# Kernel optimization log

Measured on AMD Instinct MI355X. Metric: run time of the kernel, lower is better.

Reference implementation:

```python
import jax, jax.numpy as jnp
import numpy as np

N_NODES = 50000
N_EDGES = 800000
N_GRAPHS = 64
D_IN = 768
D_HID = 256


def gcn_conv(x, src, dst, W, b, n_nodes):
    """PyG GCNConv: symmetric-normalized aggregation with self-loops.
    out = D^{-1/2} (A + I) D^{-1/2} (x @ W) + b
    """
    h = x @ W  # [N, C_out]
    # degree from target nodes, counting the implicit self-loop (+1)
    deg = jax.ops.segment_sum(jnp.ones((src.shape[0],), h.dtype), dst,
                              num_segments=n_nodes) + 1.0
    dinv = jax.lax.rsqrt(deg)  # deg >= 1 always (self-loop)
    norm = (dinv[src] * dinv[dst])[:, None]  # [E, 1]
    agg = jax.ops.segment_sum(h[src] * norm, dst, num_segments=n_nodes)
    # self-loop contribution: norm_ii = dinv_i^2
    agg = agg + (dinv * dinv)[:, None] * h
    return agg + b


def global_mean_pool(x, batch, n_graphs):
    s = jax.ops.segment_sum(x, batch, num_segments=n_graphs)
    cnt = jax.ops.segment_sum(jnp.ones((x.shape[0],), x.dtype), batch,
                              num_segments=n_graphs)
    return s / jnp.maximum(cnt, 1.0)[:, None]


def setup_inputs() -> dict:
    key = jax.random.key(0)
    ks = jax.random.split(key, 12)
    x = jax.random.normal(ks[0], (N_NODES, D_IN), jnp.float32)
    edge_index = jax.random.randint(ks[1], (2, N_EDGES), 0, N_NODES, jnp.int64)
    batch = jnp.sort(jax.random.randint(ks[2], (N_NODES,), 0, N_GRAPHS, jnp.int64))
    def glorot(k, shape):
        lim = np.sqrt(6.0 / (shape[0] + shape[1]))
        return jax.random.uniform(k, shape, jnp.float32, -lim, lim)
    return {
        "x": x, "edge_index": edge_index, "batch": batch,
        "W1": glorot(ks[3], (D_IN, D_HID)), "b1": jnp.zeros((D_HID,), jnp.float32),
        "W2": glorot(ks[4], (D_HID, D_HID)), "b2": jnp.zeros((D_HID,), jnp.float32),
        "W3": glorot(ks[5], (D_HID, D_HID)), "b3": jnp.zeros((D_HID,), jnp.float32),
        "Wl": glorot(ks[6], (D_HID, D_IN)), "bl": jnp.zeros((D_IN,), jnp.float32),
    }


def reference(x, edge_index, batch, W1, b1, W2, b2, W3, b3, Wl, bl):
    src, dst = edge_index[0], edge_index[1]
    n = x.shape[0]
    # dropout is identity in eval mode
    h = jax.nn.relu(gcn_conv(x, src, dst, W1, b1, n))
    h = jax.nn.relu(gcn_conv(h, src, dst, W2, b2, n))
    h = gcn_conv(h, src, dst, W3, b3, n)
    g = global_mean_pool(h, batch, N_GRAPHS)  # [G, D_HID]
    return g @ Wl + bl  # [G, D_IN]
```

## Files before the change

### kernel.cpp

```cpp
#include <hip/hip_runtime.h>
#include <hip/hip_bf16.h>

#define D_IN 768
#define D_HID 256

typedef __attribute__((ext_vector_type(8))) short short8;
typedef __attribute__((ext_vector_type(4))) float f32x4;

__device__ inline float b2f(unsigned short u) {
    unsigned x = ((unsigned)u) << 16;
    union { unsigned u; float f; } c; c.u = x; return c.f;
}


__global__ void k_count(const int* __restrict__ dst, int* __restrict__ deg, int E) {
    int i = blockIdx.x * 256 + threadIdx.x;
    if (i < E) atomicAdd(&deg[dst[i]], 1);
}

__global__ void k_dinv(const int* __restrict__ deg, float* __restrict__ dinv, int N) {
    int i = blockIdx.x * 256 + threadIdx.x;
    if (i < N) dinv[i] = rsqrtf((float)deg[i] + 1.0f);
}

__global__ __launch_bounds__(1024) void k_scan(const int* __restrict__ deg,
                                               int* __restrict__ row_ptr, int N) {
    __shared__ int wsum[16];
    __shared__ int carry_s;
    int t = threadIdx.x;
    int lane = t & 63, wid = t >> 6;
    if (t == 0) carry_s = 0;
    __syncthreads();
    for (int base = 0; base < N; base += 1024) {
        int i = base + t;
        int v = (i < N) ? deg[i] : 0;
        int s = v;
        #pragma unroll
        for (int d = 1; d < 64; d <<= 1) {
            int tmp = __shfl_up(s, d);
            if (lane >= d) s += tmp;
        }
        if (lane == 63) wsum[wid] = s;
        __syncthreads();
        if (wid == 0 && lane < 16) {
            int ws = wsum[lane];
            #pragma unroll
            for (int d = 1; d < 16; d <<= 1) {
                int tmp = __shfl_up(ws, d);
                if (lane >= d) ws += tmp;
            }
            wsum[lane] = ws;
        }
        __syncthreads();
        int carry = carry_s;
        int woff = (wid > 0) ? wsum[wid - 1] : 0;
        if (i < N) row_ptr[i] = carry + woff + s - v;
        __syncthreads();
        if (t == 0) carry_s = carry + wsum[15];
        __syncthreads();
    }
    if (t == 0) row_ptr[N] = carry_s;
}

__global__ void k_fill(const int* __restrict__ src, const int* __restrict__ dst,
                       const int* __restrict__ row_ptr, int* __restrict__ wptr,
                       int* __restrict__ csr_src, int E) {
    int i = blockIdx.x * 256 + threadIdx.x;
    if (i < E) {
        int d = dst[i];
        int w = atomicAdd(&wptr[d], 1);
        csr_src[row_ptr[d] + w] = src[i];
    }
}

__global__ void k_bounds(const int* __restrict__ batch, int* __restrict__ cnt,
                         int* __restrict__ offg, int N, int G) {
    int g = threadIdx.x;
    if (g >= G) return;
    auto lower = [&](int key) {
        int lo = 0, hi = N;
        while (lo < hi) {
            int mid = (lo + hi) >> 1;
            if (batch[mid] < key) lo = mid + 1; else hi = mid;
        }
        return lo;
    };
    int lo = lower(g);
    int hi = lower(g + 1);
    offg[g] = lo;
    cnt[g] = hi - lo;
}

__global__ void k_prep_B(const float* __restrict__ B, short* __restrict__ Bp, int K) {
    int t = blockIdx.x * 256 + threadIdx.x;
    if (t >= K * 256) return;
    int k = t >> 8, n = t & 255;
    float v = B[(size_t)k * 256 + n];
    __hip_bfloat16 h = __float2bfloat16(v);
    float hf = __bfloat162float(h);
    float r = v - hf;
    __hip_bfloat16 l = __float2bfloat16(r);
    int c = k >> 5, q = (k >> 3) & 3, j = k & 7;
    size_t oh = ((size_t)(c * 2 + 0) * 4 + q) * 2048 + n * 8 + j;
    size_t ol = ((size_t)(c * 2 + 1) * 4 + q) * 2048 + n * 8 + j;
    Bp[oh] = *(short*)&h;
    Bp[ol] = *(short*)&l;
}

__global__ __launch_bounds__(256) void k_gemm_mfma(const float* __restrict__ A,
                                                   const short* __restrict__ Bp,
                                                   unsigned short* __restrict__ C,
                                                   int M, int K) {
    __shared__ short Bs[16384];
    int t = threadIdx.x;
    int lane = t & 63, w = t >> 6;
    int ln = lane & 15, q = lane >> 4;
    int bm = blockIdx.x * 64;
    int m_g = bm + w * 16 + ln;
    bool valid = m_g < M;
    const float* Arow = A + (size_t)(valid ? m_g : 0) * K;

    f32x4 acc[16];
    #pragma unroll
    for (int i = 0; i < 16; ++i) acc[i] = (f32x4){0.f, 0.f, 0.f, 0.f};

    int nchunks = K >> 5;
    for (int c = 0; c < nchunks; ++c) {
        __syncthreads();
        {
            const short* srcp = Bp + (size_t)c * 16384;
            #pragma unroll
            for (int i = 0; i < 8; ++i) {
                int s = (t + i * 256) * 8;
                *(short8*)&Bs[s] = *(const short8*)&srcp[s];
            }
        }
        float av[8];
        if (valid) {
            float4 v0 = *(const float4*)&Arow[c * 32 + q * 8];
            float4 v1 = *(const float4*)&Arow[c * 32 + q * 8 + 4];
            av[0] = v0.x; av[1] = v0.y; av[2] = v0.z; av[3] = v0.w;
            av[4] = v1.x; av[5] = v1.y; av[6] = v1.z; av[7] = v1.w;
        } else {
            #pragma unroll
            for (int i = 0; i < 8; ++i) av[i] = 0.f;
        }
        short8 a_hi, a_lo;
        #pragma unroll
        for (int i = 0; i < 8; ++i) {
            __hip_bfloat16 h = __float2bfloat16(av[i]);
            float hf = __bfloat162float(h);
            __hip_bfloat16 l = __float2bfloat16(av[i] - hf);
            a_hi[i] = *(short*)&h;
            a_lo[i] = *(short*)&l;
        }
        __syncthreads();
        #pragma unroll
        for (int tt = 0; tt < 16; ++tt) {
            short8 b_hi = *(const short8*)&Bs[(0 * 4 + q) * 2048 + (tt * 16 + ln) * 8];
            short8 b_lo = *(const short8*)&Bs[(1 * 4 + q) * 2048 + (tt * 16 + ln) * 8];
            acc[tt] = __builtin_amdgcn_mfma_f32_16x16x32_bf16(a_hi, b_hi, acc[tt], 0, 0, 0);
            acc[tt] = __builtin_amdgcn_mfma_f32_16x16x32_bf16(a_hi, b_lo, acc[tt], 0, 0, 0);
            acc[tt] = __builtin_amdgcn_mfma_f32_16x16x32_bf16(a_lo, b_hi, acc[tt], 0, 0, 0);
        }
    }
    #pragma unroll
    for (int tt = 0; tt < 16; ++tt) {
        #pragma unroll
        for (int r = 0; r < 4; ++r) {
            int row = bm + w * 16 + q * 4 + r;
            if (row < M) {
                __hip_bfloat16 h = __float2bfloat16(acc[tt][r]);
                C[(size_t)row * 256 + tt * 16 + ln] = *(unsigned short*)&h;
            }
        }
    }
}

template <int RELU>
__global__ __launch_bounds__(256) void k_agg(const unsigned short* __restrict__ hin,
                                             float* __restrict__ hout,
                                             const int* __restrict__ row_ptr,
                                             const int* __restrict__ csr_src,
                                             const float* __restrict__ dinv,
                                             const float* __restrict__ bias, int N) {
    int w = threadIdx.x >> 6;
    int lane = threadIdx.x & 63;
    int row = blockIdx.x * 4 + w;
    if (row >= N) return;
    int c4 = lane * 4;
    int s = row_ptr[row], e = row_ptr[row + 1];
    float a0 = 0.f, a1 = 0.f, a2 = 0.f, a3 = 0.f;
    int j = s;
    for (; j + 4 <= e; j += 4) {
        int u0 = csr_src[j], u1 = csr_src[j + 1], u2 = csr_src[j + 2], u3 = csr_src[j + 3];
        float d0 = dinv[u0], d1 = dinv[u1], d2 = dinv[u2], d3 = dinv[u3];
        ushort4 v0 = *(const ushort4*)&hin[(size_t)u0 * 256 + c4];
        ushort4 v1 = *(const ushort4*)&hin[(size_t)u1 * 256 + c4];
        ushort4 v2 = *(const ushort4*)&hin[(size_t)u2 * 256 + c4];
        ushort4 v3 = *(const ushort4*)&hin[(size_t)u3 * 256 + c4];
        a0 += d0 * b2f(v0.x) + d1 * b2f(v1.x) + d2 * b2f(v2.x) + d3 * b2f(v3.x);
        a1 += d0 * b2f(v0.y) + d1 * b2f(v1.y) + d2 * b2f(v2.y) + d3 * b2f(v3.y);
        a2 += d0 * b2f(v0.z) + d1 * b2f(v1.z) + d2 * b2f(v2.z) + d3 * b2f(v3.z);
        a3 += d0 * b2f(v0.w) + d1 * b2f(v1.w) + d2 * b2f(v2.w) + d3 * b2f(v3.w);
    }
    for (; j < e; ++j) {
        int u = csr_src[j];
        float d = dinv[u];
        ushort4 v = *(const ushort4*)&hin[(size_t)u * 256 + c4];
        a0 += d * b2f(v.x); a1 += d * b2f(v.y); a2 += d * b2f(v.z); a3 += d * b2f(v.w);
    }
    float di = dinv[row];
    float dii = di * di;
    ushort4 vs = *(const ushort4*)&hin[(size_t)row * 256 + c4];
    float4 bb = *(const float4*)&bias[c4];
    a0 = a0 * di + dii * b2f(vs.x) + bb.x;
    a1 = a1 * di + dii * b2f(vs.y) + bb.y;
    a2 = a2 * di + dii * b2f(vs.z) + bb.z;
    a3 = a3 * di + dii * b2f(vs.w) + bb.w;
    if (RELU) {
        a0 = fmaxf(a0, 0.f); a1 = fmaxf(a1, 0.f);
        a2 = fmaxf(a2, 0.f); a3 = fmaxf(a3, 0.f);
    }
    *(float4*)&hout[(size_t)row * 256 + c4] = make_float4(a0, a1, a2, a3);
}

__global__ __launch_bounds__(256) void k_pool(const float* __restrict__ h,
                                              const int* __restrict__ cnt,
                                              const int* __restrict__ offg,
                                              float* __restrict__ g) {
    int gi = blockIdx.x, slice = blockIdx.y;
    int c = threadIdx.x;
    int start = offg[gi], n = cnt[gi];
    int per = (n + (int)gridDim.y - 1) / (int)gridDim.y;
    int r0 = slice * per;
    int r1 = min(n, r0 + per);
    float acc = 0.f;
    for (int r = r0; r < r1; ++r) acc += h[(size_t)(start + r) * D_HID + c];
    if (r1 > r0) atomicAdd(&g[gi * D_HID + c], acc);
}

__global__ __launch_bounds__(256) void k_final(const float* __restrict__ g,
                                               const int* __restrict__ cnt,
                                               const float* __restrict__ Wl,
                                               const float* __restrict__ bl,
                                               float* __restrict__ out) {
    __shared__ float gs[D_HID];
    int t = threadIdx.x;
    int gi = blockIdx.y;
    int c = blockIdx.x * 256 + t;
    float inv = 1.0f / (float)max(cnt[gi], 1);
    gs[t] = g[gi * D_HID + t] * inv;
    __syncthreads();
    float acc = bl[c];
    #pragma unroll 8
    for (int k = 0; k < D_HID; ++k) acc = fmaf(gs[k], Wl[(size_t)k * D_IN + c], acc);
    out[(size_t)gi * D_IN + c] = acc;
}


extern "C" void kernel_launch(void* const* d_in, const int* in_sizes, int n_in,
                              void* d_out, int out_size, void* d_ws, size_t ws_size,
                              hipStream_t stream) {
    const float* x     = (const float*)d_in[0];
    const int*   ei    = (const int*)d_in[1];
    const int*   batch = (const int*)d_in[2];
    const float* W1 = (const float*)d_in[3];
    const float* b1 = (const float*)d_in[4];
    const float* W2 = (const float*)d_in[5];
    const float* b2 = (const float*)d_in[6];
    const float* W3 = (const float*)d_in[7];
    const float* b3 = (const float*)d_in[8];
    const float* Wl = (const float*)d_in[9];
    const float* bl = (const float*)d_in[10];
    float* out = (float*)d_out;

    int N = in_sizes[2];
    int E = in_sizes[1] / 2;
    int G = out_size / D_IN;
    const int* srcp = ei;
    const int* dstp = ei + E;

    char* ws = (char*)d_ws;
    size_t o = 0;
    auto alloc = [&](size_t bytes) -> char* {
        char* p = ws + o;
        o += (bytes + 255) & ~(size_t)255;
        return p;
    };
    int*   deg     = (int*)alloc((size_t)N * 4);
    int*   wptr    = (int*)alloc((size_t)N * 4);
    int*   row_ptr = (int*)alloc((size_t)(N + 1) * 4);
    int*   cnt     = (int*)alloc((size_t)G * 4);
    int*   offg    = (int*)alloc((size_t)G * 4);
    int*   csr_src = (int*)alloc((size_t)E * 4);
    float* dinv    = (float*)alloc((size_t)N * 4);
    float* gbuf    = (float*)alloc((size_t)G * D_HID * 4);
    unsigned short* hA = (unsigned short*)alloc((size_t)N * D_HID * 2);
    float* hB      = (float*)alloc((size_t)N * D_HID * 4);
    short* Bp1     = (short*)alloc((size_t)D_IN * 512 * 2);
    short* Bp2     = (short*)alloc((size_t)D_HID * 512 * 2);
    short* Bp3     = (short*)alloc((size_t)D_HID * 512 * 2);

    hipMemsetAsync(deg, 0, (size_t)N * 4, stream);
    hipMemsetAsync(wptr, 0, (size_t)N * 4, stream);
    hipMemsetAsync(gbuf, 0, (size_t)G * D_HID * 4, stream);

    int gE = (E + 255) / 256;
    int gN = (N + 255) / 256;

    k_count<<<gE, 256, 0, stream>>>(dstp, deg, E);
    k_dinv<<<gN, 256, 0, stream>>>(deg, dinv, N);
    k_scan<<<1, 1024, 0, stream>>>(deg, row_ptr, N);
    k_fill<<<gE, 256, 0, stream>>>(srcp, dstp, row_ptr, wptr, csr_src, E);
    k_bounds<<<1, 64, 0, stream>>>(batch, cnt, offg, N, G);

    k_prep_B<<<D_IN, 256, 0, stream>>>(W1, Bp1, D_IN);
    k_prep_B<<<D_HID, 256, 0, stream>>>(W2, Bp2, D_HID);
    k_prep_B<<<D_HID, 256, 0, stream>>>(W3, Bp3, D_HID);

    int gemm_grid = (N + 63) / 64;
    int agg_grid = (N + 3) / 4;

    k_gemm_mfma<<<gemm_grid, 256, 0, stream>>>(x, Bp1, hA, N, D_IN);
    k_agg<1><<<agg_grid, 256, 0, stream>>>(hA, hB, row_ptr, csr_src, dinv, b1, N);
    k_gemm_mfma<<<gemm_grid, 256, 0, stream>>>(hB, Bp2, hA, N, D_HID);
    k_agg<1><<<agg_grid, 256, 0, stream>>>(hA, hB, row_ptr, csr_src, dinv, b2, N);
    k_gemm_mfma<<<gemm_grid, 256, 0, stream>>>(hB, Bp3, hA, N, D_HID);
    k_agg<0><<<agg_grid, 256, 0, stream>>>(hA, hB, row_ptr, csr_src, dinv, b3, N);

    dim3 pool_grid(G, 8);
    k_pool<<<pool_grid, 256, 0, stream>>>(hB, cnt, offg, gbuf);
    dim3 fin_grid(D_IN / 256, G);
    k_final<<<fin_grid, 256, 0, stream>>>(gbuf, cnt, Wl, bl, out);
}
```

Before: 861.3 us.

## Restructure GEMM into single-wave bf16 split passes with bf16 intermediate activations

Replaces the 256-thread shared-memory GEMM with a 64-thread kernel that reads B straight from global memory. Each wave computes 64 rows by 128 columns, with the output columns split over a second grid dimension. Layer 1 runs three passes over K (hi*hi, lo*hi, hi*lo) and truncates to get the hi part. Layers 2 and 3 use bf16 activations written directly by the aggregation kernel, so they run only two passes and need no A split. This cuts activation memory traffic and MFMA count, at the cost of lower precision for layers 2-3 and reloading A per pass.

Result: slower. 971.8 us (+12.8%).

```diff
diff --git a/kernel.cpp b/kernel.cpp
--- a/kernel.cpp
+++ b/kernel.cpp
@@ -6,10 +6,23 @@
 
 typedef __attribute__((ext_vector_type(8))) short short8;
 typedef __attribute__((ext_vector_type(4))) float f32x4;
+typedef __attribute__((ext_vector_type(4))) unsigned int u32x4;
 
 __device__ inline float b2f(unsigned short u) {
     unsigned x = ((unsigned)u) << 16;
     union { unsigned u; float f; } c; c.u = x; return c.f;
+}
+__device__ inline unsigned short f2b(float v) {
+    __hip_bfloat16 h = __float2bfloat16(v);
+    return *(unsigned short*)&h;
+}
+__device__ inline short trunc_hi(float v) {
+    unsigned u = __builtin_bit_cast(unsigned, v);
+    return (short)(u >> 16);
+}
+__device__ inline float hi_f(float v) {
+    unsigned u = __builtin_bit_cast(unsigned, v) & 0xffff0000u;
+    return __builtin_bit_cast(float, u);
 }
 
 
@@ -91,95 +104,98 @@
     cnt[g] = hi - lo;
 }
 
-__global__ void k_prep_B(const float* __restrict__ B, short* __restrict__ Bp, int K) {
+__global__ void k_prep_B2(const float* __restrict__ W, short* __restrict__ Bp, int KA) {
     int t = blockIdx.x * 256 + threadIdx.x;
-    if (t >= K * 256) return;
+    if (t >= KA * 256) return;
     int k = t >> 8, n = t & 255;
-    float v = B[(size_t)k * 256 + n];
-    __hip_bfloat16 h = __float2bfloat16(v);
-    float hf = __bfloat162float(h);
-    float r = v - hf;
-    __hip_bfloat16 l = __float2bfloat16(r);
+    float v = W[(size_t)k * 256 + n];
+    unsigned short h = f2b(v);
+    unsigned short l = f2b(v - b2f(h));
     int c = k >> 5, q = (k >> 3) & 3, j = k & 7;
-    size_t oh = ((size_t)(c * 2 + 0) * 4 + q) * 2048 + n * 8 + j;
-    size_t ol = ((size_t)(c * 2 + 1) * 4 + q) * 2048 + n * 8 + j;
-    Bp[oh] = *(short*)&h;
-    Bp[ol] = *(short*)&l;
-}
-
-__global__ __launch_bounds__(256) void k_gemm_mfma(const float* __restrict__ A,
-                                                   const short* __restrict__ Bp,
-                                                   unsigned short* __restrict__ C,
-                                                   int M, int K) {
-    __shared__ short Bs[16384];
-    int t = threadIdx.x;
-    int lane = t & 63, w = t >> 6;
+    int halfn = n >> 7, nn = n & 127;
+    size_t off = ((size_t)(c * 2 + halfn) * 4 + q) * 1024 + nn * 8 + j;
+    size_t PLANE = (size_t)(KA / 32) * 2 * 4096;
+    Bp[off] = (short)h;
+    Bp[PLANE + off] = (short)l;
+}
+
+template <int MODE>
+__global__ __launch_bounds__(64, 2) void k_gemm3(const void* __restrict__ Av,
+                                                 const short* __restrict__ Bp,
+                                                 unsigned short* __restrict__ C,
+                                                 int M) {
+    constexpr int KA = (MODE == 1) ? D_IN : D_HID;
+    constexpr int NCH = KA / 32;
+    constexpr int NPASS = (MODE == 1) ? 3 : 2;
+    constexpr int PLANE = NCH * 2 * 4096;
+    int lane = threadIdx.x;
     int ln = lane & 15, q = lane >> 4;
     int bm = blockIdx.x * 64;
-    int m_g = bm + w * 16 + ln;
-    bool valid = m_g < M;
-    const float* Arow = A + (size_t)(valid ? m_g : 0) * K;
-
-    f32x4 acc[16];
+    int half = blockIdx.y;
+
+    f32x4 acc[4][8];
     #pragma unroll
-    for (int i = 0; i < 16; ++i) acc[i] = (f32x4){0.f, 0.f, 0.f, 0.f};
-
-    int nchunks = K >> 5;
-    for (int c = 0; c < nchunks; ++c) {
-        __syncthreads();
-        {
-            const short* srcp = Bp + (size_t)c * 16384;
-            #pragma unroll
-            for (int i = 0; i < 8; ++i) {
-                int s = (t + i * 256) * 8;
-                *(short8*)&Bs[s] = *(const short8*)&srcp[s];
+    for (int s = 0; s < 4; ++s)
+        #pragma unroll
+        for (int tt = 0; tt < 8; ++tt) acc[s][tt] = (f32x4){0.f, 0.f, 0.f, 0.f};
+
+    int rbase[4]; bool rowok[4];
+    #pragma unroll
+    for (int s = 0; s < 4; ++s) { rbase[s] = bm + s * 16 + ln; rowok[s] = rbase[s] < M; }
+
+    #pragma unroll
+    for (int p = 0; p < NPASS; ++p) {
+        const short* Bb = Bp + ((MODE == 1) ? ((p == 2) ? PLANE : 0) : p * PLANE);
+        for (int cc = 0; cc < NCH; ++cc) {
+            short8 a[4];
+            #pragma unroll
+            for (int s = 0; s < 4; ++s) {
+                if (MODE == 1) {
+                    const float* Af = (const float*)Av + (size_t)rbase[s] * KA + cc * 32 + q * 8;
+                    f32x4 v0 = (f32x4){0.f, 0.f, 0.f, 0.f}, v1 = v0;
+                    if (rowok[s]) {
+                        v0 = __builtin_bit_cast(f32x4, __builtin_nontemporal_load((const u32x4*)Af));
+                        v1 = __builtin_bit_cast(f32x4, __builtin_nontemporal_load((const u32x4*)(Af + 4)));
+                    }
+                    float vv[8] = {v0[0], v0[1], v0[2], v0[3], v1[0], v1[1], v1[2], v1[3]};
+                    #pragma unroll
+                    for (int j = 0; j < 8; ++j)
+                        a[s][j] = (p == 1) ? (short)f2b(vv[j] - hi_f(vv[j])) : trunc_hi(vv[j]);
+                } else {
+                    const unsigned short* Ab =
+                        (const unsigned short*)Av + (size_t)rbase[s] * KA + cc * 32 + q * 8;
+                    short8 av = (short8){0, 0, 0, 0, 0, 0, 0, 0};
+                    if (rowok[s])
+                        av = __builtin_bit_cast(short8, __builtin_nontemporal_load((const u32x4*)Ab));
+                    a[s] = av;
+                }
             }
+            const short* bb = Bb + (size_t)(cc * 2 + half) * 4096 + q * 1024 + ln * 8;
+            short8 b[8];
+            #pragma unroll
+            for (int tt = 0; tt < 8; ++tt) b[tt] = *(const short8*)(bb + tt * 128);
+            #pragma unroll
+            for (int tt = 0; tt < 8; ++tt)
+                #pragma unroll
+                for (int s = 0; s < 4; ++s)
+                    acc[s][tt] = __builtin_amdgcn_mfma_f32_16x16x32_bf16(a[s], b[tt], acc[s][tt], 0, 0, 0);
         }
-        float av[8];
-        if (valid) {
-            float4 v0 = *(const float4*)&Arow[c * 32 + q * 8];
-            float4 v1 = *(const float4*)&Arow[c * 32 + q * 8 + 4];
-            av[0] = v0.x; av[1] = v0.y; av[2] = v0.z; av[3] = v0.w;
-            av[4] = v1.x; av[5] = v1.y; av[6] = v1.z; av[7] = v1.w;
-        } else {
-            #pragma unroll
-            for (int i = 0; i < 8; ++i) av[i] = 0.f;
-        }
-        short8 a_hi, a_lo;
+    }
+    #pragma unroll
+    for (int s = 0; s < 4; ++s)
         #pragma unroll
-        for (int i = 0; i < 8; ++i) {
-            __hip_bfloat16 h = __float2bfloat16(av[i]);
-            float hf = __bfloat162float(h);
-            __hip_bfloat16 l = __float2bfloat16(av[i] - hf);
-            a_hi[i] = *(short*)&h;
-            a_lo[i] = *(short*)&l;
-        }
-        __syncthreads();
-        #pragma unroll
-        for (int tt = 0; tt < 16; ++tt) {
-            short8 b_hi = *(const short8*)&Bs[(0 * 4 + q) * 2048 + (tt * 16 + ln) * 8];
-            short8 b_lo = *(const short8*)&Bs[(1 * 4 + q) * 2048 + (tt * 16 + ln) * 8];
-            acc[tt] = __builtin_amdgcn_mfma_f32_16x16x32_bf16(a_hi, b_hi, acc[tt], 0, 0, 0);
-            acc[tt] = __builtin_amdgcn_mfma_f32_16x16x32_bf16(a_hi, b_lo, acc[tt], 0, 0, 0);
-            acc[tt] = __builtin_amdgcn_mfma_f32_16x16x32_bf16(a_lo, b_hi, acc[tt], 0, 0, 0);
-        }
-    }
-    #pragma unroll
-    for (int tt = 0; tt < 16; ++tt) {
-        #pragma unroll
-        for (int r = 0; r < 4; ++r) {
-            int row = bm + w * 16 + q * 4 + r;
-            if (row < M) {
-                __hip_bfloat16 h = __float2bfloat16(acc[tt][r]);
-                C[(size_t)row * 256 + tt * 16 + ln] = *(unsigned short*)&h;
+        for (int tt = 0; tt < 8; ++tt)
+            #pragma unroll
+            for (int r = 0; r < 4; ++r) {
+                int row = bm + s * 16 + q * 4 + r;
+                if (row < M)
+                    C[(size_t)row * 256 + half * 128 + tt * 16 + ln] = f2b(acc[s][tt][r]);
             }
-        }
-    }
-}
-
-template <int RELU>
+}
+
+template <int RELU, int OUTBF>
 __global__ __launch_bounds__(256) void k_agg(const unsigned short* __restrict__ hin,
-                                             float* __restrict__ hout,
+                                             void* __restrict__ hout,
                                              const int* __restrict__ row_ptr,
                                              const int* __restrict__ csr_src,
                                              const float* __restrict__ dinv,
@@ -222,7 +238,12 @@
         a0 = fmaxf(a0, 0.f); a1 = fmaxf(a1, 0.f);
         a2 = fmaxf(a2, 0.f); a3 = fmaxf(a3, 0.f);
     }
-    *(float4*)&hout[(size_t)row * 256 + c4] = make_float4(a0, a1, a2, a3);
+    if (OUTBF) {
+        ushort4 o; o.x = f2b(a0); o.y = f2b(a1); o.z = f2b(a2); o.w = f2b(a3);
+        *(ushort4*)((unsigned short*)hout + (size_t)row * 256 + c4) = o;
+    } else {
+        *(float4*)((float*)hout + (size_t)row * 256 + c4) = make_float4(a0, a1, a2, a3);
+    }
 }
 
 __global__ __launch_bounds__(256) void k_pool(const float* __restrict__ h,
@@ -296,11 +317,12 @@
     int*   csr_src = (int*)alloc((size_t)E * 4);
     float* dinv    = (float*)alloc((size_t)N * 4);
     float* gbuf    = (float*)alloc((size_t)G * D_HID * 4);
-    unsigned short* hA = (unsigned short*)alloc((size_t)N * D_HID * 2);
-    float* hB      = (float*)alloc((size_t)N * D_HID * 4);
-    short* Bp1     = (short*)alloc((size_t)D_IN * 512 * 2);
-    short* Bp2     = (short*)alloc((size_t)D_HID * 512 * 2);
-    short* Bp3     = (short*)alloc((size_t)D_HID * 512 * 2);
+    unsigned short* hG  = (unsigned short*)alloc((size_t)N * D_HID * 2);
+    unsigned short* hA2 = (unsigned short*)alloc((size_t)N * D_HID * 2);
+    float* hF      = (float*)alloc((size_t)N * D_HID * 4);
+    short* Bp1     = (short*)alloc((size_t)(D_IN / 32) * 2 * 4096 * 2 * 2);
+    short* Bp2     = (short*)alloc((size_t)(D_HID / 32) * 2 * 4096 * 2 * 2);
+    short* Bp3     = (short*)alloc((size_t)(D_HID / 32) * 2 * 4096 * 2 * 2);
 
     hipMemsetAsync(deg, 0, (size_t)N * 4, stream);
     hipMemsetAsync(wptr, 0, (size_t)N * 4, stream);
@@ -315,22 +337,22 @@
     k_fill<<<gE, 256, 0, stream>>>(srcp, dstp, row_ptr, wptr, csr_src, E);
     k_bounds<<<1, 64, 0, stream>>>(batch, cnt, offg, N, G);
 
-    k_prep_B<<<D_IN, 256, 0, stream>>>(W1, Bp1, D_IN);
-    k_prep_B<<<D_HID, 256, 0, stream>>>(W2, Bp2, D_HID);
-    k_prep_B<<<D_HID, 256, 0, stream>>>(W3, Bp3, D_HID);
-
-    int gemm_grid = (N + 63) / 64;
+    k_prep_B2<<<D_IN, 256, 0, stream>>>(W1, Bp1, D_IN);
+    k_prep_B2<<<D_HID, 256, 0, stream>>>(W2, Bp2, D_HID);
+    k_prep_B2<<<D_HID, 256, 0, stream>>>(W3, Bp3, D_HID);
+
+    dim3 gemm_grid((N + 63) / 64, 2);
     int agg_grid = (N + 3) / 4;
 
-    k_gemm_mfma<<<gemm_grid, 256, 0, stream>>>(x, Bp1, hA, N, D_IN);
-    k_agg<1><<<agg_grid, 256, 0, stream>>>(hA, hB, row_ptr, csr_src, dinv, b1, N);
-    k_gemm_mfma<<<gemm_grid, 256, 0, stream>>>(hB, Bp2, hA, N, D_HID);
-    k_agg<1><<<agg_grid, 256, 0, stream>>>(hA, hB, row_ptr, csr_src, dinv, b2, N);
-    k_gemm_mfma<<<gemm_grid, 256, 0, stream>>>(hB, Bp3, hA, N, D_HID);
-    k_agg<0><<<agg_grid, 256, 0, stream>>>(hA, hB, row_ptr, csr_src, dinv, b3, N);
+    k_gemm3<1><<<gemm_grid, 64, 0, stream>>>(x, Bp1, hG, N);
+    k_agg<1, 1><<<agg_grid, 256, 0, stream>>>(hG, hA2, row_ptr, csr_src, dinv, b1, N);
+    k_gemm3<2><<<gemm_grid, 64, 0, stream>>>(hA2, Bp2, hG, N);
+    k_agg<1, 1><<<agg_grid, 256, 0, stream>>>(hG, hA2, row_ptr, csr_src, dinv, b2, N);
+    k_gemm3<2><<<gemm_grid, 64, 0, stream>>>(hA2, Bp3, hG, N);
+    k_agg<0, 0><<<agg_grid, 256, 0, stream>>>(hG, hF, row_ptr, csr_src, dinv, b3, N);
 
     dim3 pool_grid(G, 8);
-    k_pool<<<pool_grid, 256, 0, stream>>>(hB, cnt, offg, gbuf);
+    k_pool<<<pool_grid, 256, 0, stream>>>(hF, cnt, offg, gbuf);
     dim3 fin_grid(D_IN / 256, G);
     k_final<<<fin_grid, 256, 0, stream>>>(gbuf, cnt, Wl, bl, out);
 }
```
